# Kernel tuning notes

Measured on AMD Instinct MI355X. Metric: run time of the kernel, lower is better.

The kernel has to match this reference:

```python
import jax, jax.numpy as jnp
import numpy as np

B, T, ENC, DEC, ATTN = 64, 2048, 512, 512, 256


def setup_inputs() -> dict:
    key = jax.random.key(0)
    k1, k2, k3, k4, k5, k6 = jax.random.split(key, 6)
    enc_out = jax.random.normal(k1, (B, T, ENC), dtype=jnp.float32)
    dec_hidden = jax.random.normal(k2, (B, DEC), dtype=jnp.float32)
    mask = jax.random.randint(k3, (B, T), 0, 2) == 1  # True = masked out
    # learned params (Linear with bias=False); torch Linear weight is [out,in],
    # we store transposed [in,out] for x @ W convention
    s_enc = 1.0 / np.sqrt(ENC)
    s_dec = 1.0 / np.sqrt(DEC)
    s_v = 1.0 / np.sqrt(ATTN)
    W_enc = jax.random.uniform(k4, (ENC, ATTN), jnp.float32, -s_enc, s_enc)
    W_dec = jax.random.uniform(k5, (DEC, ATTN), jnp.float32, -s_dec, s_dec)
    v = jax.random.uniform(k6, (ATTN,), jnp.float32, -s_v, s_v)
    return {"enc_out": enc_out, "dec_hidden": dec_hidden, "mask": mask,
            "W_enc": W_enc, "W_dec": W_dec, "v": v}


def reference(enc_out, dec_hidden, mask, W_enc, W_dec, v):
    # proj_enc: [B,T,A]; proj_dec: [B,1,A]
    proj_enc = jnp.einsum('bte,ea->bta', enc_out, W_enc)
    proj_dec = jnp.einsum('bd,da->ba', dec_hidden, W_dec)[:, None, :]
    # energy: [B,T] -- additive (Bahdanau) score
    energy = jnp.einsum('bta,a->bt', jnp.tanh(proj_enc + proj_dec), v)
    energy = jnp.where(mask, -jnp.inf, energy)
    attn_w = jax.nn.softmax(energy, axis=-1)
    attn_w = jnp.nan_to_num(attn_w, nan=0.0)  # fully-masked rows -> 0
    context = jnp.einsum('bt,bte->be', attn_w, enc_out)
    return context, attn_w
```

## Files before the change

### kernel.cpp

```cpp
#include <hip/hip_runtime.h>
#include <stdint.h>

#define Bx 64
#define Tx 2048
#define ENCx 512
#define ATTx 256

typedef float f4 __attribute__((ext_vector_type(4)));
typedef float f32x4 __attribute__((ext_vector_type(4)));
typedef short bf16x8 __attribute__((ext_vector_type(8)));

__device__ __forceinline__ unsigned short f2bf(float f) {
  union { float f; uint32_t u; } c; c.f = f;
  uint32_t u = c.u;
  u += 0x7fffu + ((u >> 16) & 1u);
  return (unsigned short)(u >> 16);
}

__device__ __forceinline__ uint32_t pk_bf(float lo, float hi) {
  uint32_t a = __float_as_uint(lo) + 0x8000u;
  uint32_t b = __float_as_uint(hi) + 0x8000u;
  return __builtin_amdgcn_perm(b, a, 0x07060302u);
}

__device__ __forceinline__ float ftanh(float x) {
  x = fminf(8.f, fmaxf(-8.f, x));
  float z = __expf(2.f * x);
  return 1.f - __fdividef(2.f, z + 1.f);
}

__global__ void k0_wt(const float* __restrict__ W, unsigned short* __restrict__ WTc) {
  int tid = blockIdx.x * 256 + threadIdx.x;
  int kc = tid >> 13;
  int r = tid & 8191;
  int n = r >> 5;
  int kk = r & 31;
  WTc[tid] = f2bf(W[(kc * 32 + kk) * ATTx + n]);
}

__global__ void k1_pd(const float* __restrict__ dec, const float* __restrict__ Wd,
                      float* __restrict__ pd) {
  __shared__ float ld[512];
  int b = blockIdx.x, a = threadIdx.x;
  ld[a] = dec[b * 512 + a];
  ld[a + 256] = dec[b * 512 + a + 256];
  __syncthreads();
  float s = 0.f;
#pragma unroll 8
  for (int d = 0; d < 512; ++d) s = fmaf(ld[d], Wd[d * ATTx + a], s);
  pd[b * ATTx + a] = s;
}

__global__ __launch_bounds__(256) void k2_energy(
    const float* __restrict__ enc, const unsigned short* __restrict__ WTc,
    const float* __restrict__ pd, const float* __restrict__ v,
    const int* __restrict__ mask, float* __restrict__ energy) {
  __shared__ float pdv[256];
  __shared__ float vvs[256];
  const int tid = threadIdx.x;
  const int wid = tid >> 6;
  const int lane = tid & 63;
  const int q = lane >> 4;
  const int c15 = lane & 15;
  const int m0 = blockIdx.x * 128;
  const int b = m0 >> 11;

  pdv[tid] = pd[b * ATTx + tid];
  vvs[tid] = v[tid];
  __syncthreads();

  const int mrow = m0 + wid * 32 + c15;
  const float* a0p = enc + (size_t)mrow * ENCx + q * 8;
  const float* a1p = a0p + 16 * ENCx;
  const unsigned short* wb = WTc + c15 * 32 + q * 8;

  f32x4 acc[2][16];
#pragma unroll
  for (int mt = 0; mt < 2; ++mt)
#pragma unroll
    for (int ct = 0; ct < 16; ++ct) { f32x4 z = {0.f,0.f,0.f,0.f}; acc[mt][ct] = z; }

  for (int kc = 0; kc < 16; ++kc) {
    f4 x0 = *(const f4*)(a0p + kc * 32);
    f4 x1 = *(const f4*)(a0p + kc * 32 + 4);
    f4 y0 = *(const f4*)(a1p + kc * 32);
    f4 y1 = *(const f4*)(a1p + kc * 32 + 4);
    bf16x8 bfr[16];
    const unsigned short* wkc = wb + kc * 8192;
#pragma unroll
    for (int ct = 0; ct < 16; ++ct)
      bfr[ct] = *(const bf16x8*)(wkc + ct * 512);

    union { uint32_t u[4]; bf16x8 v; } am0, am1;
    am0.u[0] = pk_bf(x0.x, x0.y); am0.u[1] = pk_bf(x0.z, x0.w);
    am0.u[2] = pk_bf(x1.x, x1.y); am0.u[3] = pk_bf(x1.z, x1.w);
    am1.u[0] = pk_bf(y0.x, y0.y); am1.u[1] = pk_bf(y0.z, y0.w);
    am1.u[2] = pk_bf(y1.x, y1.y); am1.u[3] = pk_bf(y1.z, y1.w);

#pragma unroll
    for (int ct = 0; ct < 16; ++ct) {
      acc[0][ct] = __builtin_amdgcn_mfma_f32_16x16x32_bf16(am0.v, bfr[ct], acc[0][ct], 0, 0, 0);
      acc[1][ct] = __builtin_amdgcn_mfma_f32_16x16x32_bf16(am1.v, bfr[ct], acc[1][ct], 0, 0, 0);
    }
  }

  float ps[2][4];
#pragma unroll
  for (int mt = 0; mt < 2; ++mt)
#pragma unroll
    for (int i = 0; i < 4; ++i) ps[mt][i] = 0.f;
#pragma unroll
  for (int ct = 0; ct < 16; ++ct) {
    float pv = pdv[ct * 16 + c15];
    float vv = vvs[ct * 16 + c15];
#pragma unroll
    for (int mt = 0; mt < 2; ++mt)
#pragma unroll
      for (int i = 0; i < 4; ++i)
        ps[mt][i] += ftanh(acc[mt][ct][i] + pv) * vv;
  }
#pragma unroll
  for (int s = 1; s < 16; s <<= 1)
#pragma unroll
    for (int mt = 0; mt < 2; ++mt)
#pragma unroll
      for (int i = 0; i < 4; ++i)
        ps[mt][i] += __shfl_xor(ps[mt][i], s, 64);
  if (c15 == 0) {
#pragma unroll
    for (int mt = 0; mt < 2; ++mt)
#pragma unroll
      for (int i = 0; i < 4; ++i) {
        int gm = m0 + wid * 32 + mt * 16 + q * 4 + i;
        energy[gm] = mask[gm] ? -1e30f : ps[mt][i];
      }
  }
}

__global__ void k3_softmax(const float* __restrict__ energy, float* __restrict__ attn) {
  __shared__ float redm[4];
  __shared__ float redl[4];
  int b = blockIdx.x, tid = threadIdx.x;
  int lane = tid & 63, wid = tid >> 6;
  float e[8];
#pragma unroll
  for (int i = 0; i < 8; ++i) e[i] = energy[b * Tx + tid + i * 256];
  float m = e[0];
#pragma unroll
  for (int i = 1; i < 8; ++i) m = fmaxf(m, e[i]);
#pragma unroll
  for (int s = 1; s < 64; s <<= 1) m = fmaxf(m, __shfl_xor(m, s, 64));
  if (lane == 0) redm[wid] = m;
  __syncthreads();
  m = fmaxf(fmaxf(redm[0], redm[1]), fmaxf(redm[2], redm[3]));
  bool dead = (m < -1e29f);
  float w[8];
  float l = 0.f;
#pragma unroll
  for (int i = 0; i < 8; ++i) { w[i] = dead ? 0.f : __expf(e[i] - m); l += w[i]; }
#pragma unroll
  for (int s = 1; s < 64; s <<= 1) l += __shfl_xor(l, s, 64);
  if (lane == 0) redl[wid] = l;
  __syncthreads();
  l = redl[0] + redl[1] + redl[2] + redl[3];
  float inv = dead ? 0.f : __fdividef(1.f, l);
#pragma unroll
  for (int i = 0; i < 8; ++i) attn[b * Tx + tid + i * 256] = w[i] * inv;
}

__global__ void k4_ctx(const float* __restrict__ enc, const float* __restrict__ attn,
                       float* __restrict__ part) {
  __shared__ float wl[128];
  __shared__ f4 comb[128];
  int tc = blockIdx.x & 15, b = blockIdx.x >> 4;
  int tid = threadIdx.x;
  if (tid < 128) wl[tid] = attn[b * Tx + tc * 128 + tid];
  __syncthreads();
  int tl = tid >> 7;
  int ef = tid & 127;
  f4 a = {0.f, 0.f, 0.f, 0.f};
  const f4* base = (const f4*)(enc + ((size_t)b * Tx + tc * 128) * ENCx) + ef;
  for (int t = tl; t < 128; t += 2) {
    f4 x = base[(size_t)t * 128];
    a += x * wl[t];
  }
  if (tl == 1) comb[ef] = a;
  __syncthreads();
  if (tl == 0) {
    a += comb[ef];
    *((f4*)(part + ((size_t)tc * 64 + b) * 512) + ef) = a;
  }
}

__global__ void k5_red(const float* __restrict__ part, float* __restrict__ ctx) {
  int idx = blockIdx.x * 256 + threadIdx.x;
  float s = 0.f;
#pragma unroll
  for (int tc = 0; tc < 16; ++tc) s += part[tc * 32768 + idx];
  ctx[idx] = s;
}

extern "C" void kernel_launch(void* const* d_in, const int* in_sizes, int n_in,
                              void* d_out, int out_size, void* d_ws, size_t ws_size,
                              hipStream_t stream) {
  const float* enc   = (const float*)d_in[0];
  const float* dec   = (const float*)d_in[1];
  const int*   mask  = (const int*)d_in[2];
  const float* W_enc = (const float*)d_in[3];
  const float* W_dec = (const float*)d_in[4];
  const float* v     = (const float*)d_in[5];
  float* ctx  = (float*)d_out;
  float* attn = ctx + Bx * ENCx;
  char* ws = (char*)d_ws;
  unsigned short* WTc = (unsigned short*)ws;
  float* pd     = (float*)(ws + 262144);
  float* energy = (float*)(ws + 262144 + 65536);
  float* part   = (float*)(ws + 262144 + 65536 + 524288);

  k0_wt<<<512, 256, 0, stream>>>(W_enc, WTc);
  k1_pd<<<64, 256, 0, stream>>>(dec, W_dec, pd);
  k2_energy<<<1024, 256, 0, stream>>>(enc, WTc, pd, v, mask, energy);
  k3_softmax<<<64, 256, 0, stream>>>(energy, attn);
  k4_ctx<<<1024, 256, 0, stream>>>(enc, attn, part);
  k5_red<<<128, 256, 0, stream>>>(part, ctx);
}
```

Measured before the change: 487.6 us.

## Fuse energy, local softmax and context accumulation using fp16 LDS-staged encoder tiles

Result: faster. 466.1 us (-4.4%).

```diff
diff --git a/kernel.cpp b/kernel.cpp
--- a/kernel.cpp
+++ b/kernel.cpp
@@ -9,6 +9,7 @@
 typedef float f4 __attribute__((ext_vector_type(4)));
 typedef float f32x4 __attribute__((ext_vector_type(4)));
 typedef short bf16x8 __attribute__((ext_vector_type(8)));
+typedef __fp16 h2 __attribute__((ext_vector_type(2)));
 
 __device__ __forceinline__ unsigned short f2bf(float f) {
   union { float f; uint32_t u; } c; c.f = f;
@@ -21,6 +22,12 @@
   uint32_t a = __float_as_uint(lo) + 0x8000u;
   uint32_t b = __float_as_uint(hi) + 0x8000u;
   return __builtin_amdgcn_perm(b, a, 0x07060302u);
+}
+
+__device__ __forceinline__ uint32_t pk_f16(float lo, float hi) {
+  h2 r = __builtin_amdgcn_cvt_pkrtz(lo, hi);
+  union { h2 h; uint32_t u; } c; c.h = r;
+  return c.u;
 }
 
 __device__ __forceinline__ float ftanh(float x) {
@@ -51,45 +58,74 @@
   pd[b * ATTx + a] = s;
 }
 
-__global__ __launch_bounds__(256) void k2_energy(
+__global__ __launch_bounds__(128, 1) void k2_fused(
     const float* __restrict__ enc, const unsigned short* __restrict__ WTc,
     const float* __restrict__ pd, const float* __restrict__ v,
-    const int* __restrict__ mask, float* __restrict__ energy) {
+    const int* __restrict__ mask, float* __restrict__ energy,
+    float* __restrict__ part, float* __restrict__ mloc, float* __restrict__ lloc) {
   __shared__ float pdv[256];
   __shared__ float vvs[256];
+  __shared__ unsigned short enc_s[64 * 512];
+  __shared__ float e_lds[64];
+  __shared__ float wl[64];
+
   const int tid = threadIdx.x;
   const int wid = tid >> 6;
   const int lane = tid & 63;
   const int q = lane >> 4;
   const int c15 = lane & 15;
-  const int m0 = blockIdx.x * 128;
+  const int m0 = blockIdx.x * 64;
   const int b = m0 >> 11;
+  const int chunk = blockIdx.x & 31;
 
   pdv[tid] = pd[b * ATTx + tid];
+  pdv[tid + 128] = pd[b * ATTx + tid + 128];
   vvs[tid] = v[tid];
-  __syncthreads();
-
-  const int mrow = m0 + wid * 32 + c15;
+  vvs[tid + 128] = v[tid + 128];
+  __syncthreads();
+
+  const int r0 = wid * 32 + c15;
+  const int mrow = m0 + r0;
   const float* a0p = enc + (size_t)mrow * ENCx + q * 8;
   const float* a1p = a0p + 16 * ENCx;
   const unsigned short* wb = WTc + c15 * 32 + q * 8;
 
+  uint4* enc16 = (uint4*)enc_s;
+  const int sw = r0 & 7;
+  const int w0base = r0 * 64 + q;
+  const int w1base = (r0 + 16) * 64 + q;
+
   f32x4 acc[2][16];
 #pragma unroll
   for (int mt = 0; mt < 2; ++mt)
 #pragma unroll
     for (int ct = 0; ct < 16; ++ct) { f32x4 z = {0.f,0.f,0.f,0.f}; acc[mt][ct] = z; }
 
+  f4 x0 = *(const f4*)(a0p);
+  f4 x1 = *(const f4*)(a0p + 4);
+  f4 y0 = *(const f4*)(a1p);
+  f4 y1 = *(const f4*)(a1p + 4);
+
   for (int kc = 0; kc < 16; ++kc) {
-    f4 x0 = *(const f4*)(a0p + kc * 32);
-    f4 x1 = *(const f4*)(a0p + kc * 32 + 4);
-    f4 y0 = *(const f4*)(a1p + kc * 32);
-    f4 y1 = *(const f4*)(a1p + kc * 32 + 4);
     bf16x8 bfr[16];
     const unsigned short* wkc = wb + kc * 8192;
 #pragma unroll
     for (int ct = 0; ct < 16; ++ct)
       bfr[ct] = *(const bf16x8*)(wkc + ct * 512);
+
+    const int kn = (kc < 15) ? kc + 1 : 15;
+    f4 nx0 = *(const f4*)(a0p + kn * 32);
+    f4 nx1 = *(const f4*)(a0p + kn * 32 + 4);
+    f4 ny0 = *(const f4*)(a1p + kn * 32);
+    f4 ny1 = *(const f4*)(a1p + kn * 32 + 4);
+
+    uint4 hp0, hp1;
+    hp0.x = pk_f16(x0.x, x0.y); hp0.y = pk_f16(x0.z, x0.w);
+    hp0.z = pk_f16(x1.x, x1.y); hp0.w = pk_f16(x1.z, x1.w);
+    hp1.x = pk_f16(y0.x, y0.y); hp1.y = pk_f16(y0.z, y0.w);
+    hp1.z = pk_f16(y1.x, y1.y); hp1.w = pk_f16(y1.z, y1.w);
+    enc16[(w0base + kc * 4) ^ sw] = hp0;
+    enc16[(w1base + kc * 4) ^ sw] = hp1;
 
     union { uint32_t u[4]; bf16x8 v; } am0, am1;
     am0.u[0] = pk_bf(x0.x, x0.y); am0.u[1] = pk_bf(x0.z, x0.w);
@@ -102,6 +138,7 @@
       acc[0][ct] = __builtin_amdgcn_mfma_f32_16x16x32_bf16(am0.v, bfr[ct], acc[0][ct], 0, 0, 0);
       acc[1][ct] = __builtin_amdgcn_mfma_f32_16x16x32_bf16(am1.v, bfr[ct], acc[1][ct], 0, 0, 0);
     }
+    x0 = nx0; x1 = nx1; y0 = ny0; y1 = ny1;
   }
 
   float ps[2][4];
@@ -131,17 +168,58 @@
     for (int mt = 0; mt < 2; ++mt)
 #pragma unroll
       for (int i = 0; i < 4; ++i) {
-        int gm = m0 + wid * 32 + mt * 16 + q * 4 + i;
-        energy[gm] = mask[gm] ? -1e30f : ps[mt][i];
+        int lr = wid * 32 + mt * 16 + q * 4 + i;
+        int gm = m0 + lr;
+        float ev = mask[gm] ? -1e30f : ps[mt][i];
+        energy[gm] = ev;
+        e_lds[lr] = ev;
       }
   }
-}
-
-__global__ void k3_softmax(const float* __restrict__ energy, float* __restrict__ attn) {
+  __syncthreads();
+
+  float ev = e_lds[lane];
+  float mx = ev;
+#pragma unroll
+  for (int s = 1; s < 64; s <<= 1) mx = fmaxf(mx, __shfl_xor(mx, s, 64));
+  float w = (ev < -1e29f) ? 0.f : __expf(ev - mx);
+  float ls = w;
+#pragma unroll
+  for (int s = 1; s < 64; s <<= 1) ls += __shfl_xor(ls, s, 64);
+  if (wid == 0) wl[lane] = w;
+  if (tid == 0) { mloc[b * 32 + chunk] = mx; lloc[b * 32 + chunk] = ls; }
+  __syncthreads();
+
+  const uint32_t* encu = (const uint32_t*)enc_s;
+  float a0 = 0.f, a1 = 0.f, a2 = 0.f, a3 = 0.f;
+#pragma unroll 4
+  for (int t = 0; t < 64; ++t) {
+    float wv = wl[t];
+    int xr = (t & 7) << 2;
+    uint32_t p0 = encu[(t * 256 + tid) ^ xr];
+    uint32_t p1 = encu[(t * 256 + tid + 128) ^ xr];
+    union { uint32_t u; h2 h; } c0, c1;
+    c0.u = p0; c1.u = p1;
+    a0 = fmaf((float)c0.h.x, wv, a0);
+    a1 = fmaf((float)c0.h.y, wv, a1);
+    a2 = fmaf((float)c1.h.x, wv, a2);
+    a3 = fmaf((float)c1.h.y, wv, a3);
+  }
+  float* pp = part + (size_t)(chunk * 64 + b) * 512;
+  float2 s0; s0.x = a0; s0.y = a1;
+  float2 s1; s1.x = a2; s1.y = a3;
+  *(float2*)(pp + 2 * tid) = s0;
+  *(float2*)(pp + 2 * tid + 256) = s1;
+}
+
+__global__ void k3_merge(const float* __restrict__ energy, const float* __restrict__ part,
+                         const float* __restrict__ mloc, const float* __restrict__ lloc,
+                         float* __restrict__ attn, float* __restrict__ ctx) {
   __shared__ float redm[4];
   __shared__ float redl[4];
+  __shared__ float sc[32];
   int b = blockIdx.x, tid = threadIdx.x;
   int lane = tid & 63, wid = tid >> 6;
+
   float e[8];
 #pragma unroll
   for (int i = 0; i < 8; ++i) e[i] = energy[b * Tx + tid + i * 256];
@@ -166,38 +244,31 @@
   float inv = dead ? 0.f : __fdividef(1.f, l);
 #pragma unroll
   for (int i = 0; i < 8; ++i) attn[b * Tx + tid + i * 256] = w[i] * inv;
-}
-
-__global__ void k4_ctx(const float* __restrict__ enc, const float* __restrict__ attn,
-                       float* __restrict__ part) {
-  __shared__ float wl[128];
-  __shared__ f4 comb[128];
-  int tc = blockIdx.x & 15, b = blockIdx.x >> 4;
-  int tid = threadIdx.x;
-  if (tid < 128) wl[tid] = attn[b * Tx + tc * 128 + tid];
-  __syncthreads();
-  int tl = tid >> 7;
-  int ef = tid & 127;
-  f4 a = {0.f, 0.f, 0.f, 0.f};
-  const f4* base = (const f4*)(enc + ((size_t)b * Tx + tc * 128) * ENCx) + ef;
-  for (int t = tl; t < 128; t += 2) {
-    f4 x = base[(size_t)t * 128];
-    a += x * wl[t];
-  }
-  if (tl == 1) comb[ef] = a;
-  __syncthreads();
-  if (tl == 0) {
-    a += comb[ef];
-    *((f4*)(part + ((size_t)tc * 64 + b) * 512) + ef) = a;
-  }
-}
-
-__global__ void k5_red(const float* __restrict__ part, float* __restrict__ ctx) {
-  int idx = blockIdx.x * 256 + threadIdx.x;
-  float s = 0.f;
-#pragma unroll
-  for (int tc = 0; tc < 16; ++tc) s += part[tc * 32768 + idx];
-  ctx[idx] = s;
+
+  if (tid < 64) {
+    float mc = (lane < 32) ? mloc[b * 32 + lane] : -3e38f;
+    float lc = (lane < 32) ? lloc[b * 32 + lane] : 0.f;
+    float mg = mc;
+#pragma unroll
+    for (int s = 1; s < 64; s <<= 1) mg = fmaxf(mg, __shfl_xor(mg, s, 64));
+    float sl = (lane < 32) ? lc * __expf(mc - mg) : 0.f;
+    float lg = sl;
+#pragma unroll
+    for (int s = 1; s < 64; s <<= 1) lg += __shfl_xor(lg, s, 64);
+    float ig = (lg > 0.f) ? __fdividef(1.f, lg) : 0.f;
+    if (lane < 32) sc[lane] = __expf(mc - mg) * ig;
+  }
+  __syncthreads();
+  float2 a; a.x = 0.f; a.y = 0.f;
+  const float* pb = part + (size_t)b * 512 + tid * 2;
+#pragma unroll 8
+  for (int c = 0; c < 32; ++c) {
+    float2 p = *(const float2*)(pb + (size_t)c * 64 * 512);
+    float s = sc[c];
+    a.x = fmaf(p.x, s, a.x);
+    a.y = fmaf(p.y, s, a.y);
+  }
+  *(float2*)(ctx + b * 512 + tid * 2) = a;
 }
 
 extern "C" void kernel_launch(void* const* d_in, const int* in_sizes, int n_in,
@@ -215,12 +286,12 @@
   unsigned short* WTc = (unsigned short*)ws;
   float* pd     = (float*)(ws + 262144);
   float* energy = (float*)(ws + 262144 + 65536);
-  float* part   = (float*)(ws + 262144 + 65536 + 524288);
+  float* part   = (float*)(ws + 851968);
+  float* mloc   = (float*)(ws + 851968 + 4194304);
+  float* lloc   = (float*)(ws + 851968 + 4194304 + 8192);
 
   k0_wt<<<512, 256, 0, stream>>>(W_enc, WTc);
   k1_pd<<<64, 256, 0, stream>>>(dec, W_dec, pd);
-  k2_energy<<<1024, 256, 0, stream>>>(enc, WTc, pd, v, mask, energy);
-  k3_softmax<<<64, 256, 0, stream>>>(energy, attn);
-  k4_ctx<<<1024, 256, 0, stream>>>(enc, attn, part);
-  k5_red<<<128, 256, 0, stream>>>(part, ctx);
-}
+  k2_fused<<<2048, 128, 0, stream>>>(enc, WTc, pd, v, mask, energy, part, mloc, lloc);
+  k3_merge<<<64, 256, 0, stream>>>(energy, part, mloc, lloc, attn, ctx);
+}
```
